# Performance work log

Hardware: AMD Instinct MI355X
Metric: run time of the kernel (lower is better)

The kernel has to match this reference:

```python
import jax, jax.numpy as jnp
import numpy as np

D_MODEL = 32   # channels arg = Mamba d_model
D_INNER = 32   # expand=1
D_STATE = 8
DT_RANK = 2    # ceil(32/16)
D_CONV = 4


def layer_norm(h, g, b, eps=1e-5):
    m = jnp.mean(h, axis=-1, keepdims=True)
    v = jnp.var(h, axis=-1, keepdims=True)
    return (h - m) * jax.lax.rsqrt(v + eps) * g + b


def causal_conv1d(h, w, b):
    # h: [B, d, L]; w: [d, K] depthwise; torch Conv1d(padding=K-1) truncated to first L
    out = jax.lax.conv_general_dilated(h, w[:, None, :], (1,), [(D_CONV - 1, 0)],
                                       dimension_numbers=('NCH', 'OIH', 'NCH'),
                                       feature_group_count=h.shape[1])
    return out + b[None, :, None]


def selective_scan(u, delta, A, Bm, Cm, D):
    # u, delta: [B, d, L]; A: [d, n]; Bm, Cm: [B, n, L]; D: [d]
    dA = jnp.exp(jnp.einsum('bdl,dn->lbdn', delta, A))       # [L, B, d, n]
    dBu = jnp.einsum('bdl,bnl,bdl->lbdn', delta, Bm, u)      # [L, B, d, n]
    Cseq = jnp.transpose(Cm, (2, 0, 1))                      # [L, B, n]
    h0 = jnp.zeros((u.shape[0], A.shape[0], A.shape[1]), u.dtype)

    def step(h, inp):
        dA_t, dBu_t, C_t = inp
        h = dA_t * h + dBu_t
        return h, jnp.einsum('bdn,bn->bd', h, C_t)

    _, ys = jax.lax.scan(step, h0, (dA, dBu, Cseq))          # ys: [L, B, d]
    return jnp.transpose(ys, (1, 2, 0)) + D[None, :, None] * u


def mamba_direction(xz, conv_w, conv_b, xproj_w, dtproj_w, dtproj_b, A_log, D):
    xh, z = jnp.split(xz, 2, axis=1)                         # each [B, d_inner, L]
    xh = jax.nn.silu(causal_conv1d(xh, conv_w, conv_b))
    x_dbl = jnp.einsum('bdl,kd->bkl', xh, xproj_w)           # [B, dt_rank+2n, L]
    dt, Bm, Cm = jnp.split(x_dbl, [DT_RANK, DT_RANK + D_STATE], axis=1)
    dt = jax.nn.softplus(jnp.einsum('brl,dr->bdl', dt, dtproj_w) + dtproj_b[None, :, None])
    y = selective_scan(xh, dt, -jnp.exp(A_log), Bm, Cm, D)
    return y * jax.nn.silu(z)


def forward(x, lin1_w, lin1_b, ln1_g, ln1_b, in_proj_w,
            conv_w_f, conv_b_f, xproj_w_f, dtproj_w_f, dtproj_b_f, A_log_f, D_f,
            conv_w_r, conv_b_r, xproj_w_r, dtproj_w_r, dtproj_b_r, A_log_r, D_r,
            out_proj_w, mnorm_g, mnorm_b, lin2_w, lin2_b):
    avg = jnp.mean(x, axis=(2, 3))                           # [B, C] adaptive avg pool
    mx = jnp.max(x, axis=(2, 3))                             # [B, C] adaptive max pool
    combined = jnp.stack([avg, mx], axis=-1)                 # [B, C, 2]
    h = combined @ lin1_w.T + lin1_b                         # [B, C, d_model]
    h = layer_norm(h, ln1_g, ln1_b)
    # bidirectional Mamba (bimamba v2) over sequence length L = C
    xz = jnp.einsum('blc,ec->bel', h, in_proj_w)             # [B, 2*d_inner, L]
    out_f = mamba_direction(xz, conv_w_f, conv_b_f, xproj_w_f, dtproj_w_f, dtproj_b_f, A_log_f, D_f)
    out_r = mamba_direction(xz[..., ::-1], conv_w_r, conv_b_r, xproj_w_r, dtproj_w_r, dtproj_b_r, A_log_r, D_r)[..., ::-1]
    out = (out_f + out_r) / 2.0                              # if_devide_out=True
    out = jnp.einsum('bdl,od->blo', out, out_proj_w)         # [B, L, d_model]
    out = layer_norm(out, mnorm_g, mnorm_b)                  # use_norm=True
    att = jax.nn.sigmoid(out @ lin2_w.T + lin2_b)            # [B, L, 1]
    return att[..., None] * 0.25 + 0.875                     # [B, C, 1, 1]


def setup_inputs() -> dict:
    key = jax.random.key(0)
    ks = jax.random.split(key, 12)
    B, C, H, W = 32, 512, 64, 64

    def rn(k, shape, s):
        return jax.random.normal(k, shape, jnp.float32) * s

    A_log = jnp.log(jnp.broadcast_to(jnp.arange(1, D_STATE + 1, dtype=jnp.float32), (D_INNER, D_STATE)))
    return {
        'x': jax.random.normal(ks[0], (B, C, H, W), jnp.float32),
        'lin1_w': rn(ks[1], (D_MODEL, 2), 0.5),
        'lin1_b': jnp.zeros((D_MODEL,), jnp.float32),
        'ln1_g': jnp.ones((D_MODEL,), jnp.float32),
        'ln1_b': jnp.zeros((D_MODEL,), jnp.float32),
        'in_proj_w': rn(ks[2], (2 * D_INNER, D_MODEL), 0.1),
        'conv_w_f': rn(ks[3], (D_INNER, D_CONV), 0.3),
        'conv_b_f': jnp.zeros((D_INNER,), jnp.float32),
        'xproj_w_f': rn(ks[4], (DT_RANK + 2 * D_STATE, D_INNER), 0.1),
        'dtproj_w_f': rn(ks[5], (D_INNER, DT_RANK), 0.5),
        'dtproj_b_f': jnp.full((D_INNER,), -4.6, jnp.float32),
        'A_log_f': A_log,
        'D_f': jnp.ones((D_INNER,), jnp.float32),
        'conv_w_r': rn(ks[6], (D_INNER, D_CONV), 0.3),
        'conv_b_r': jnp.zeros((D_INNER,), jnp.float32),
        'xproj_w_r': rn(ks[7], (DT_RANK + 2 * D_STATE, D_INNER), 0.1),
        'dtproj_w_r': rn(ks[8], (D_INNER, DT_RANK), 0.5),
        'dtproj_b_r': jnp.full((D_INNER,), -4.6, jnp.float32),
        'A_log_r': A_log,
        'D_r': jnp.ones((D_INNER,), jnp.float32),
        'out_proj_w': rn(ks[9], (D_MODEL, D_INNER), 0.1),
        'mnorm_g': jnp.ones((D_MODEL,), jnp.float32),
        'mnorm_b': jnp.zeros((D_MODEL,), jnp.float32),
        'lin2_w': rn(ks[10], (1, D_MODEL), 0.3),
        'lin2_b': jnp.zeros((1,), jnp.float32),
    }


def reference(x, lin1_w, lin1_b, ln1_g, ln1_b, in_proj_w,
              conv_w_f, conv_b_f, xproj_w_f, dtproj_w_f, dtproj_b_f, A_log_f, D_f,
              conv_w_r, conv_b_r, xproj_w_r, dtproj_w_r, dtproj_b_r, A_log_r, D_r,
              out_proj_w, mnorm_g, mnorm_b, lin2_w, lin2_b):
    return forward(x, lin1_w, lin1_b, ln1_g, ln1_b, in_proj_w,
                   conv_w_f, conv_b_f, xproj_w_f, dtproj_w_f, dtproj_b_f, A_log_f, D_f,
                   conv_w_r, conv_b_r, xproj_w_r, dtproj_w_r, dtproj_b_r, A_log_r, D_r,
                   out_proj_w, mnorm_g, mnorm_b, lin2_w, lin2_b)
```

## Files before the change

kernel.cpp:

```cpp
#include <hip/hip_runtime.h>
#include <math.h>

#define BB 32
#define CC 512
#define HW 4096
#define DM 32
#define DI 32
#define DS 8
#define KC 4

#define NCH 16
#define CHL 32

__device__ __forceinline__ float siluf(float x) {
    return x / (1.0f + __expf(-x));
}
__device__ __forceinline__ float softplusf(float x) {
    float ax = fabsf(x);
    return fmaxf(x, 0.0f) + log1pf(__expf(-ax));
}

__global__ __launch_bounds__(256) void poolproj_kernel(
    const float* __restrict__ x,
    const float* __restrict__ lin1_w, const float* __restrict__ lin1_b,
    const float* __restrict__ ln1_g, const float* __restrict__ ln1_b,
    const float* __restrict__ in_proj_w, float* __restrict__ xz)
{
    int bc = blockIdx.x;
    int b = bc >> 9, l = bc & 511;
    const float4* xp = reinterpret_cast<const float4*>(x + (size_t)bc * HW);
    int tid = threadIdx.x;

    __shared__ float sWp[64][33];
    __shared__ float ss[4], sm[4];
    __shared__ float h_s[DM];

    float s = 0.f, m = -INFINITY;
#pragma unroll
    for (int r = 0; r < 4; ++r) {
        float4 v = xp[r * 256 + tid];
        s += (v.x + v.y) + (v.z + v.w);
        m = fmaxf(m, fmaxf(fmaxf(v.x, v.y), fmaxf(v.z, v.w)));
    }
    for (int i = tid; i < 64 * DM; i += 256) sWp[i >> 5][i & 31] = in_proj_w[i];

    for (int off = 32; off > 0; off >>= 1) {
        s += __shfl_down(s, off);
        m = fmaxf(m, __shfl_down(m, off));
    }
    int wave = tid >> 6;
    if ((tid & 63) == 0) { ss[wave] = s; sm[wave] = m; }
    __syncthreads();

    if (tid < 32) {
        float S = (ss[0] + ss[1]) + (ss[2] + ss[3]);
        float M = fmaxf(fmaxf(sm[0], sm[1]), fmaxf(sm[2], sm[3]));
        float a = S * (1.0f / HW);
        int m_ = tid;
        float h = a * lin1_w[2 * m_] + M * lin1_w[2 * m_ + 1] + lin1_b[m_];
        float sum = h;
#pragma unroll
        for (int mask = 1; mask < 32; mask <<= 1) sum += __shfl_xor(sum, mask);
        float mean = sum * (1.0f / DM);
        float d = h - mean;
        float vs = d * d;
#pragma unroll
        for (int mask = 1; mask < 32; mask <<= 1) vs += __shfl_xor(vs, mask);
        float rs = rsqrtf(vs * (1.0f / DM) + 1e-5f);
        h_s[m_] = d * rs * ln1_g[m_] + ln1_b[m_];
    }
    __syncthreads();

    if (tid < 64) {
        int e = tid;
        float acc = 0.f;
#pragma unroll
        for (int m_ = 0; m_ < DM; ++m_) acc += h_s[m_] * sWp[e][m_];
        xz[(((size_t)b * 64 + e) << 9) + l] = acc;
    }
}

__global__ __launch_bounds__(256) void convscan1_kernel(
    const float* __restrict__ xz,
    const float* __restrict__ conv_w_f, const float* __restrict__ conv_b_f,
    const float* __restrict__ xproj_w_f, const float* __restrict__ dtproj_w_f,
    const float* __restrict__ dtproj_b_f,
    const float* __restrict__ conv_w_r, const float* __restrict__ conv_b_r,
    const float* __restrict__ xproj_w_r, const float* __restrict__ dtproj_w_r,
    const float* __restrict__ dtproj_b_r,
    const float* __restrict__ A_log_f, const float* __restrict__ A_log_r,
    float* __restrict__ u_g, float* __restrict__ dt_g,
    float* __restrict__ B_g, float* __restrict__ C_g,
    float* __restrict__ carrA, float* __restrict__ carrH)
{
    int bx = blockIdx.x;
    int bd = bx >> 4, j = bx & 15;
    int b = bd >> 1, dir = bd & 1;
    int tid = threadIdx.x;
    const float* cw = dir ? conv_w_r : conv_w_f;
    const float* cb = dir ? conv_b_r : conv_b_f;
    const float* xw = dir ? xproj_w_r : xproj_w_f;
    const float* dw = dir ? dtproj_w_r : dtproj_w_f;
    const float* db = dir ? dtproj_b_r : dtproj_b_f;
    const float* Alog = dir ? A_log_r : A_log_f;
    const float* xzb = xz + (size_t)b * 64 * 512;

    __shared__ float xt[32][39];
    __shared__ float xw_s[18][33];
    __shared__ float u_s[CHL][33];
    __shared__ float dt_s[CHL][33];
    __shared__ float B_s[CHL][9];
    __shared__ float C_s[CHL][9];
    __shared__ float dtr_s[CHL][2];

    for (int idx = tid; idx < 32 * 35; idx += 256) {
        int dd = idx / 35, t = idx - dd * 35;
        int sidx = j * CHL - 3 + t;
        float v = 0.f;
        if (sidx >= 0) {
            int orig = dir ? (511 - sidx) : sidx;
            v = xzb[(dd << 9) + orig];
        }
        xt[dd][t] = v;
    }
    for (int idx = tid; idx < 18 * 32; idx += 256)
        xw_s[idx >> 5][idx & 31] = xw[idx];
    __syncthreads();

    int l = tid >> 3, g8 = tid & 7;
#pragma unroll
    for (int i = 0; i < 4; ++i) {
        int dd = g8 * 4 + i;
        float acc = cb[dd];
#pragma unroll
        for (int k = 0; k < KC; ++k) acc += cw[dd * KC + k] * xt[dd][l + k];
        u_s[l][dd] = siluf(acc);
    }
    __syncthreads();

    for (int o = g8; o < 18; o += 8) {
        float acc = 0.f;
#pragma unroll
        for (int m_ = 0; m_ < 32; ++m_) acc += u_s[l][m_] * xw_s[o][m_];
        if (o < 2) dtr_s[l][o] = acc;
        else if (o < 10) B_s[l][o - 2] = acc;
        else             C_s[l][o - 10] = acc;
    }
    __syncthreads();

    size_t rowbase = ((size_t)bd * 512 + j * CHL) * 32;
    for (int idx = tid; idx < CHL * 32; idx += 256) {
        int ll = idx >> 5, dd = idx & 31;
        float v = dtr_s[ll][0] * dw[dd * 2] + dtr_s[ll][1] * dw[dd * 2 + 1] + db[dd];
        float sp = softplusf(v);
        dt_s[ll][dd] = sp;
        dt_g[rowbase + idx] = sp;
        u_g[rowbase + idx] = u_s[ll][dd];
    }
    size_t base8 = ((size_t)bd * 512 + j * CHL) * 8;
    if (tid < CHL * 8) {
        B_g[base8 + tid] = B_s[tid >> 3][tid & 7];
        C_g[base8 + tid] = C_s[tid >> 3][tid & 7];
    }
    __syncthreads();

    int dd = tid >> 3, nn = tid & 7;
    float Aa = -__expf(Alog[tid]);
    float ap = 1.f, h = 0.f;
#pragma unroll 4
    for (int sl = 0; sl < CHL; ++sl) {
        float dtv = dt_s[sl][dd];
        float uu  = u_s[sl][dd];
        float bm  = B_s[sl][nn];
        float dA  = __expf(dtv * Aa);
        ap *= dA;
        h = dA * h + dtv * uu * bm;
    }
    carrA[((size_t)bx << 8) + tid] = ap;
    carrH[((size_t)bx << 8) + tid] = h;
}

__global__ __launch_bounds__(128) void scan2final_kernel(
    const float* __restrict__ u_g, const float* __restrict__ dt_g,
    const float* __restrict__ B_g, const float* __restrict__ C_g,
    const float* __restrict__ carrA, const float* __restrict__ carrH,
    const float* __restrict__ A_log_f, const float* __restrict__ D_f,
    const float* __restrict__ A_log_r, const float* __restrict__ D_r,
    const float* __restrict__ xz,
    const float* __restrict__ out_proj_w, const float* __restrict__ mnorm_g,
    const float* __restrict__ mnorm_b, const float* __restrict__ lin2_w,
    const float* __restrict__ lin2_b, float* __restrict__ out)
{
    int bx = blockIdx.x;
    int b = bx >> 4, t = bx & 15;
    int tid = threadIdx.x;
    int dir = tid >> 6;
    int r = tid & 63;
    int dd = r >> 1, nh = r & 1, n0 = nh * 4;
    int bd = b * 2 + dir;
    int tt = dir ? (15 - t) : t;

    const float* Alog = dir ? A_log_r : A_log_f;
    const float* Dp   = dir ? D_r : D_f;

    float A0 = -__expf(Alog[dd * 8 + n0 + 0]);
    float A1 = -__expf(Alog[dd * 8 + n0 + 1]);
    float A2 = -__expf(Alog[dd * 8 + n0 + 2]);
    float A3 = -__expf(Alog[dd * 8 + n0 + 3]);
    float Dd = Dp[dd];

    float h0 = 0.f, h1 = 0.f, h2 = 0.f, h3 = 0.f;
    for (int jj = 0; jj < tt; ++jj) {
        size_t cbase = (((size_t)bd * NCH + jj) << 8) + dd * 8 + n0;
        float4 av = *reinterpret_cast<const float4*>(carrA + cbase);
        float4 hv = *reinterpret_cast<const float4*>(carrH + cbase);
        h0 = av.x * h0 + hv.x;
        h1 = av.y * h1 + hv.y;
        h2 = av.z * h2 + hv.z;
        h3 = av.w * h3 + hv.w;
    }

    __shared__ float y_s[2][2][CHL][33];

    size_t sb = (size_t)bd * 512 + tt * CHL;
#pragma unroll 4
    for (int sl = 0; sl < CHL; ++sl) {
        size_t s32 = (sb + sl) * 32 + dd;
        float dtv = dt_g[s32];
        float uu  = u_g[s32];
        float4 Bv = *reinterpret_cast<const float4*>(B_g + (sb + sl) * 8 + n0);
        float4 Cv = *reinterpret_cast<const float4*>(C_g + (sb + sl) * 8 + n0);
        float dtu = dtv * uu;
        h0 = __expf(dtv * A0) * h0 + dtu * Bv.x;
        h1 = __expf(dtv * A1) * h1 + dtu * Bv.y;
        h2 = __expf(dtv * A2) * h2 + dtu * Bv.z;
        h3 = __expf(dtv * A3) * h3 + dtu * Bv.w;
        float py = h0 * Cv.x + h1 * Cv.y + h2 * Cv.z + h3 * Cv.w;
        if (nh == 0) py += Dd * uu;
        int ll = dir ? (CHL - 1 - sl) : sl;
        y_s[dir][nh][ll][dd] = py;
    }
    __syncthreads();

    if (tid < CHL) {
        int lo = t * CHL + tid;
        float comb[DI];
#pragma unroll
        for (int d2 = 0; d2 < DI; ++d2) {
            float ys = y_s[0][0][tid][d2] + y_s[0][1][tid][d2]
                     + y_s[1][0][tid][d2] + y_s[1][1][tid][d2];
            float z = xz[(((size_t)(b * 64 + 32 + d2)) << 9) + lo];
            comb[d2] = 0.5f * ys * siluf(z);
        }
        float o[DM];
        float mean = 0.f;
#pragma unroll
        for (int oo = 0; oo < DM; ++oo) {
            float acc = 0.f;
#pragma unroll
            for (int d2 = 0; d2 < DI; ++d2) acc += comb[d2] * out_proj_w[oo * DI + d2];
            o[oo] = acc;
            mean += acc;
        }
        mean *= (1.0f / DM);
        float var = 0.f;
#pragma unroll
        for (int oo = 0; oo < DM; ++oo) { float df = o[oo] - mean; var += df * df; }
        var *= (1.0f / DM);
        float rs = rsqrtf(var + 1e-5f);
        float s = lin2_b[0];
#pragma unroll
        for (int oo = 0; oo < DM; ++oo) {
            float v = (o[oo] - mean) * rs * mnorm_g[oo] + mnorm_b[oo];
            s += v * lin2_w[oo];
        }
        float att = 1.0f / (1.0f + __expf(-s));
        out[(size_t)b * 512 + lo] = 0.25f * att + 0.875f;
    }
}

extern "C" void kernel_launch(void* const* d_in, const int* in_sizes, int n_in,
                              void* d_out, int out_size, void* d_ws, size_t ws_size,
                              hipStream_t stream)
{
    const float* x         = (const float*)d_in[0];
    const float* lin1_w    = (const float*)d_in[1];
    const float* lin1_b    = (const float*)d_in[2];
    const float* ln1_g     = (const float*)d_in[3];
    const float* ln1_b     = (const float*)d_in[4];
    const float* in_proj_w = (const float*)d_in[5];
    const float* conv_w_f  = (const float*)d_in[6];
    const float* conv_b_f  = (const float*)d_in[7];
    const float* xproj_w_f = (const float*)d_in[8];
    const float* dtproj_w_f= (const float*)d_in[9];
    const float* dtproj_b_f= (const float*)d_in[10];
    const float* A_log_f   = (const float*)d_in[11];
    const float* D_f       = (const float*)d_in[12];
    const float* conv_w_r  = (const float*)d_in[13];
    const float* conv_b_r  = (const float*)d_in[14];
    const float* xproj_w_r = (const float*)d_in[15];
    const float* dtproj_w_r= (const float*)d_in[16];
    const float* dtproj_b_r= (const float*)d_in[17];
    const float* A_log_r   = (const float*)d_in[18];
    const float* D_r       = (const float*)d_in[19];
    const float* out_proj_w= (const float*)d_in[20];
    const float* mnorm_g   = (const float*)d_in[21];
    const float* mnorm_b   = (const float*)d_in[22];
    const float* lin2_w    = (const float*)d_in[23];
    const float* lin2_b    = (const float*)d_in[24];

    float* ws   = (float*)d_ws;
    float* xz   = ws;
    float* u_g  = xz + 1048576;
    float* dt_g = u_g + 1048576;
    float* B_g  = dt_g + 1048576;
    float* C_g  = B_g + 262144;
    float* carrA= C_g + 262144;
    float* carrH= carrA + 262144;
    (void)ws_size; (void)in_sizes; (void)n_in; (void)out_size;

    poolproj_kernel<<<BB * CC, 256, 0, stream>>>(x, lin1_w, lin1_b, ln1_g, ln1_b, in_proj_w, xz);
    convscan1_kernel<<<BB * 2 * NCH, 256, 0, stream>>>(
        xz, conv_w_f, conv_b_f, xproj_w_f, dtproj_w_f, dtproj_b_f,
        conv_w_r, conv_b_r, xproj_w_r, dtproj_w_r, dtproj_b_r,
        A_log_f, A_log_r, u_g, dt_g, B_g, C_g, carrA, carrH);
    scan2final_kernel<<<BB * NCH, 128, 0, stream>>>(
        u_g, dt_g, B_g, C_g, carrA, carrH,
        A_log_f, D_f, A_log_r, D_r, xz,
        out_proj_w, mnorm_g, mnorm_b, lin2_w, lin2_b, (float*)d_out);
}
```

Baseline: 93.21 us.

## Pool per-wave rows, transpose xz layout, and batch carry loads in scan

The pooling kernel now launches 512 blocks, and each wave processes 8 rows of x with wave-level shuffles. This removes the 16384 tiny blocks and their block-wide syncs, and in_proj weights are loaded into shared memory once per 32 rows instead of once per row. The xz buffer layout changes from [B,64,L] to [B,L,64], so the projection writes are coalesced and the consumers read contiguous channel vectors. The carry-combine loop in the scan kernel loads four chunk carries at a time to expose memory-level parallelism. The trade-offs are fewer blocks for latency hiding in the 134MB streaming read, and transposed gather patterns in the conv kernel's load.

Measured after the change: 115.8 us. +24.3%, slower.

```diff
diff --git a/kernel.cpp b/kernel.cpp
--- a/kernel.cpp
+++ b/kernel.cpp
@@ -26,38 +26,31 @@
     const float* __restrict__ ln1_g, const float* __restrict__ ln1_b,
     const float* __restrict__ in_proj_w, float* __restrict__ xz)
 {
-    int bc = blockIdx.x;
-    int b = bc >> 9, l = bc & 511;
-    const float4* xp = reinterpret_cast<const float4*>(x + (size_t)bc * HW);
+    __shared__ float sWp[64][33];
     int tid = threadIdx.x;
-
-    __shared__ float sWp[64][33];
-    __shared__ float ss[4], sm[4];
-    __shared__ float h_s[DM];
-
-    float s = 0.f, m = -INFINITY;
-#pragma unroll
-    for (int r = 0; r < 4; ++r) {
-        float4 v = xp[r * 256 + tid];
-        s += (v.x + v.y) + (v.z + v.w);
-        m = fmaxf(m, fmaxf(fmaxf(v.x, v.y), fmaxf(v.z, v.w)));
-    }
     for (int i = tid; i < 64 * DM; i += 256) sWp[i >> 5][i & 31] = in_proj_w[i];
-
-    for (int off = 32; off > 0; off >>= 1) {
-        s += __shfl_down(s, off);
-        m = fmaxf(m, __shfl_down(m, off));
-    }
-    int wave = tid >> 6;
-    if ((tid & 63) == 0) { ss[wave] = s; sm[wave] = m; }
-    __syncthreads();
-
-    if (tid < 32) {
-        float S = (ss[0] + ss[1]) + (ss[2] + ss[3]);
-        float M = fmaxf(fmaxf(sm[0], sm[1]), fmaxf(sm[2], sm[3]));
-        float a = S * (1.0f / HW);
-        int m_ = tid;
-        float h = a * lin1_w[2 * m_] + M * lin1_w[2 * m_ + 1] + lin1_b[m_];
+    __syncthreads();
+
+    int wave = tid >> 6, lane = tid & 63;
+    int row0 = blockIdx.x * 32 + wave * 8;
+    for (int i = 0; i < 8; ++i) {
+        int row = row0 + i;
+        const float4* xp = reinterpret_cast<const float4*>(x + (size_t)row * HW);
+        float s = 0.f, mxv = -INFINITY;
+#pragma unroll
+        for (int k = 0; k < 16; ++k) {
+            float4 v = xp[k * 64 + lane];
+            s += (v.x + v.y) + (v.z + v.w);
+            mxv = fmaxf(mxv, fmaxf(fmaxf(v.x, v.y), fmaxf(v.z, v.w)));
+        }
+#pragma unroll
+        for (int off = 1; off < 64; off <<= 1) {
+            s += __shfl_xor(s, off);
+            mxv = fmaxf(mxv, __shfl_xor(mxv, off));
+        }
+        float a = s * (1.0f / HW);
+        int m_ = lane & 31;
+        float h = a * lin1_w[2 * m_] + mxv * lin1_w[2 * m_ + 1] + lin1_b[m_];
         float sum = h;
 #pragma unroll
         for (int mask = 1; mask < 32; mask <<= 1) sum += __shfl_xor(sum, mask);
@@ -67,16 +60,12 @@
 #pragma unroll
         for (int mask = 1; mask < 32; mask <<= 1) vs += __shfl_xor(vs, mask);
         float rs = rsqrtf(vs * (1.0f / DM) + 1e-5f);
-        h_s[m_] = d * rs * ln1_g[m_] + ln1_b[m_];
-    }
-    __syncthreads();
-
-    if (tid < 64) {
-        int e = tid;
+        float hn = d * rs * ln1_g[m_] + ln1_b[m_];
         float acc = 0.f;
 #pragma unroll
-        for (int m_ = 0; m_ < DM; ++m_) acc += h_s[m_] * sWp[e][m_];
-        xz[(((size_t)b * 64 + e) << 9) + l] = acc;
+        for (int mm = 0; mm < DM; ++mm)
+            acc += __shfl(hn, mm) * sWp[lane][mm];
+        xz[((size_t)row << 6) + lane] = acc;
     }
 }
 
@@ -103,7 +92,6 @@
     const float* dw = dir ? dtproj_w_r : dtproj_w_f;
     const float* db = dir ? dtproj_b_r : dtproj_b_f;
     const float* Alog = dir ? A_log_r : A_log_f;
-    const float* xzb = xz + (size_t)b * 64 * 512;
 
     __shared__ float xt[32][39];
     __shared__ float xw_s[18][33];
@@ -113,13 +101,13 @@
     __shared__ float C_s[CHL][9];
     __shared__ float dtr_s[CHL][2];
 
-    for (int idx = tid; idx < 32 * 35; idx += 256) {
-        int dd = idx / 35, t = idx - dd * 35;
+    for (int idx = tid; idx < 35 * 32; idx += 256) {
+        int t = idx >> 5, dd = idx & 31;
         int sidx = j * CHL - 3 + t;
         float v = 0.f;
         if (sidx >= 0) {
             int orig = dir ? (511 - sidx) : sidx;
-            v = xzb[(dd << 9) + orig];
+            v = xz[(((size_t)b * 512 + orig) << 6) + dd];
         }
         xt[dd][t] = v;
     }
@@ -210,14 +198,27 @@
     float Dd = Dp[dd];
 
     float h0 = 0.f, h1 = 0.f, h2 = 0.f, h3 = 0.f;
-    for (int jj = 0; jj < tt; ++jj) {
-        size_t cbase = (((size_t)bd * NCH + jj) << 8) + dd * 8 + n0;
-        float4 av = *reinterpret_cast<const float4*>(carrA + cbase);
-        float4 hv = *reinterpret_cast<const float4*>(carrH + cbase);
-        h0 = av.x * h0 + hv.x;
-        h1 = av.y * h1 + hv.y;
-        h2 = av.z * h2 + hv.z;
-        h3 = av.w * h3 + hv.w;
+    for (int g = 0; g < 4; ++g) {
+        int jbase = g * 4;
+        if (jbase >= tt) break;
+        float4 av[4], hv[4];
+#pragma unroll
+        for (int k = 0; k < 4; ++k) {
+            int jj = jbase + k;
+            int js = (jj < tt) ? jj : 0;
+            size_t cbase = (((size_t)bd * NCH + js) << 8) + dd * 8 + n0;
+            av[k] = *reinterpret_cast<const float4*>(carrA + cbase);
+            hv[k] = *reinterpret_cast<const float4*>(carrH + cbase);
+        }
+#pragma unroll
+        for (int k = 0; k < 4; ++k) {
+            if (jbase + k < tt) {
+                h0 = av[k].x * h0 + hv[k].x;
+                h1 = av[k].y * h1 + hv[k].y;
+                h2 = av[k].z * h2 + hv[k].z;
+                h3 = av[k].w * h3 + hv[k].w;
+            }
+        }
     }
 
     __shared__ float y_s[2][2][CHL][33];
@@ -244,13 +245,13 @@
 
     if (tid < CHL) {
         int lo = t * CHL + tid;
+        const float* zrow = xz + (((size_t)b * 512 + lo) << 6) + 32;
         float comb[DI];
 #pragma unroll
         for (int d2 = 0; d2 < DI; ++d2) {
             float ys = y_s[0][0][tid][d2] + y_s[0][1][tid][d2]
                      + y_s[1][0][tid][d2] + y_s[1][1][tid][d2];
-            float z = xz[(((size_t)(b * 64 + 32 + d2)) << 9) + lo];
-            comb[d2] = 0.5f * ys * siluf(z);
+            comb[d2] = 0.5f * ys * siluf(zrow[d2]);
         }
         float o[DM];
         float mean = 0.f;
@@ -319,7 +320,7 @@
     float* carrH= carrA + 262144;
     (void)ws_size; (void)in_sizes; (void)n_in; (void)out_size;
 
-    poolproj_kernel<<<BB * CC, 256, 0, stream>>>(x, lin1_w, lin1_b, ln1_g, ln1_b, in_proj_w, xz);
+    poolproj_kernel<<<512, 256, 0, stream>>>(x, lin1_w, lin1_b, ln1_g, ln1_b, in_proj_w, xz);
     convscan1_kernel<<<BB * 2 * NCH, 256, 0, stream>>>(
         xz, conv_w_f, conv_b_f, xproj_w_f, dtproj_w_f, dtproj_b_f,
         conv_w_r, conv_b_r, xproj_w_r, dtproj_w_r, dtproj_b_r,
```

## Split pooling from projection, transpose xz layout, widen final scan kernel

Applied to the files above, without the earlier changes.

The pooled reduction becomes its own lightweight kernel, and a separate projection kernel computes LayerNorm and in_proj with one wave per row. xz is stored position-major ([B, L, 64]), so the projection writes and the conv loads are coalesced. The final kernel now uses 512 threads, one per (dir, d, n): it stages u/dt/B/C/z and out_proj in shared memory, reduces over n with shuffles, and spreads the out_proj/LayerNorm/lin2 epilogue across all threads instead of 32. In exchange this adds a kernel launch and a round trip of the pooled values through global memory.

Result: faster. 86.76 us (-6.9%).

```diff
diff --git a/kernel.cpp b/kernel.cpp
--- a/kernel.cpp
+++ b/kernel.cpp
@@ -20,64 +20,66 @@
     return fmaxf(x, 0.0f) + log1pf(__expf(-ax));
 }
 
-__global__ __launch_bounds__(256) void poolproj_kernel(
-    const float* __restrict__ x,
+__global__ __launch_bounds__(256) void pool_kernel(const float* __restrict__ x,
+                                                   float* __restrict__ avg,
+                                                   float* __restrict__ mx) {
+    int bc = blockIdx.x;
+    const float4* xp = reinterpret_cast<const float4*>(x + (size_t)bc * HW);
+    int tid = threadIdx.x;
+    float s = 0.f, m = -INFINITY;
+#pragma unroll
+    for (int r = 0; r < 4; ++r) {
+        float4 v = xp[r * 256 + tid];
+        s += (v.x + v.y) + (v.z + v.w);
+        m = fmaxf(m, fmaxf(fmaxf(v.x, v.y), fmaxf(v.z, v.w)));
+    }
+    for (int off = 32; off > 0; off >>= 1) {
+        s += __shfl_down(s, off);
+        m = fmaxf(m, __shfl_down(m, off));
+    }
+    __shared__ float ss[4], sm[4];
+    int wave = tid >> 6;
+    if ((tid & 63) == 0) { ss[wave] = s; sm[wave] = m; }
+    __syncthreads();
+    if (tid == 0) {
+        float S = (ss[0] + ss[1]) + (ss[2] + ss[3]);
+        float M = fmaxf(fmaxf(sm[0], sm[1]), fmaxf(sm[2], sm[3]));
+        avg[bc] = S * (1.0f / HW);
+        mx[bc]  = M;
+    }
+}
+
+__global__ __launch_bounds__(256) void hproj_kernel(
+    const float* __restrict__ avg, const float* __restrict__ mx,
     const float* __restrict__ lin1_w, const float* __restrict__ lin1_b,
     const float* __restrict__ ln1_g, const float* __restrict__ ln1_b,
     const float* __restrict__ in_proj_w, float* __restrict__ xz)
 {
-    int bc = blockIdx.x;
-    int b = bc >> 9, l = bc & 511;
-    const float4* xp = reinterpret_cast<const float4*>(x + (size_t)bc * HW);
+    __shared__ float sWp[64][33];
     int tid = threadIdx.x;
-
-    __shared__ float sWp[64][33];
-    __shared__ float ss[4], sm[4];
-    __shared__ float h_s[DM];
-
-    float s = 0.f, m = -INFINITY;
-#pragma unroll
-    for (int r = 0; r < 4; ++r) {
-        float4 v = xp[r * 256 + tid];
-        s += (v.x + v.y) + (v.z + v.w);
-        m = fmaxf(m, fmaxf(fmaxf(v.x, v.y), fmaxf(v.z, v.w)));
-    }
     for (int i = tid; i < 64 * DM; i += 256) sWp[i >> 5][i & 31] = in_proj_w[i];
-
-    for (int off = 32; off > 0; off >>= 1) {
-        s += __shfl_down(s, off);
-        m = fmaxf(m, __shfl_down(m, off));
-    }
-    int wave = tid >> 6;
-    if ((tid & 63) == 0) { ss[wave] = s; sm[wave] = m; }
-    __syncthreads();
-
-    if (tid < 32) {
-        float S = (ss[0] + ss[1]) + (ss[2] + ss[3]);
-        float M = fmaxf(fmaxf(sm[0], sm[1]), fmaxf(sm[2], sm[3]));
-        float a = S * (1.0f / HW);
-        int m_ = tid;
-        float h = a * lin1_w[2 * m_] + M * lin1_w[2 * m_ + 1] + lin1_b[m_];
-        float sum = h;
-#pragma unroll
-        for (int mask = 1; mask < 32; mask <<= 1) sum += __shfl_xor(sum, mask);
-        float mean = sum * (1.0f / DM);
-        float d = h - mean;
-        float vs = d * d;
-#pragma unroll
-        for (int mask = 1; mask < 32; mask <<= 1) vs += __shfl_xor(vs, mask);
-        float rs = rsqrtf(vs * (1.0f / DM) + 1e-5f);
-        h_s[m_] = d * rs * ln1_g[m_] + ln1_b[m_];
-    }
-    __syncthreads();
-
-    if (tid < 64) {
-        int e = tid;
-        float acc = 0.f;
-#pragma unroll
-        for (int m_ = 0; m_ < DM; ++m_) acc += h_s[m_] * sWp[e][m_];
-        xz[(((size_t)b * 64 + e) << 9) + l] = acc;
-    }
+    __syncthreads();
+
+    int wave = tid >> 6, lane = tid & 63;
+    int row = blockIdx.x * 4 + wave;
+    float a = avg[row], M = mx[row];
+    int m_ = lane & 31;
+    float h = a * lin1_w[2 * m_] + M * lin1_w[2 * m_ + 1] + lin1_b[m_];
+    float sum = h;
+#pragma unroll
+    for (int mask = 1; mask < 32; mask <<= 1) sum += __shfl_xor(sum, mask);
+    float mean = sum * (1.0f / DM);
+    float d = h - mean;
+    float vs = d * d;
+#pragma unroll
+    for (int mask = 1; mask < 32; mask <<= 1) vs += __shfl_xor(vs, mask);
+    float rs = rsqrtf(vs * (1.0f / DM) + 1e-5f);
+    float hn = d * rs * ln1_g[m_] + ln1_b[m_];
+    float acc = 0.f;
+#pragma unroll
+    for (int mm = 0; mm < DM; ++mm)
+        acc += __shfl(hn, mm) * sWp[lane][mm];
+    xz[((size_t)row << 6) + lane] = acc;
 }
 
 __global__ __launch_bounds__(256) void convscan1_kernel(
@@ -103,7 +105,6 @@
     const float* dw = dir ? dtproj_w_r : dtproj_w_f;
     const float* db = dir ? dtproj_b_r : dtproj_b_f;
     const float* Alog = dir ? A_log_r : A_log_f;
-    const float* xzb = xz + (size_t)b * 64 * 512;
 
     __shared__ float xt[32][39];
     __shared__ float xw_s[18][33];
@@ -113,13 +114,13 @@
     __shared__ float C_s[CHL][9];
     __shared__ float dtr_s[CHL][2];
 
-    for (int idx = tid; idx < 32 * 35; idx += 256) {
-        int dd = idx / 35, t = idx - dd * 35;
+    for (int idx = tid; idx < 35 * 32; idx += 256) {
+        int t = idx >> 5, dd = idx & 31;
         int sidx = j * CHL - 3 + t;
         float v = 0.f;
         if (sidx >= 0) {
             int orig = dir ? (511 - sidx) : sidx;
-            v = xzb[(dd << 9) + orig];
+            v = xz[(((size_t)b * 512 + orig) << 6) + dd];
         }
         xt[dd][t] = v;
     }
@@ -180,7 +181,7 @@
     carrH[((size_t)bx << 8) + tid] = h;
 }
 
-__global__ __launch_bounds__(128) void scan2final_kernel(
+__global__ __launch_bounds__(512) void scan2final_kernel(
     const float* __restrict__ u_g, const float* __restrict__ dt_g,
     const float* __restrict__ B_g, const float* __restrict__ C_g,
     const float* __restrict__ carrA, const float* __restrict__ carrH,
@@ -194,88 +195,125 @@
     int bx = blockIdx.x;
     int b = bx >> 4, t = bx & 15;
     int tid = threadIdx.x;
-    int dir = tid >> 6;
-    int r = tid & 63;
-    int dd = r >> 1, nh = r & 1, n0 = nh * 4;
-    int bd = b * 2 + dir;
-    int tt = dir ? (15 - t) : t;
-
-    const float* Alog = dir ? A_log_r : A_log_f;
-    const float* Dp   = dir ? D_r : D_f;
-
-    float A0 = -__expf(Alog[dd * 8 + n0 + 0]);
-    float A1 = -__expf(Alog[dd * 8 + n0 + 1]);
-    float A2 = -__expf(Alog[dd * 8 + n0 + 2]);
-    float A3 = -__expf(Alog[dd * 8 + n0 + 3]);
-    float Dd = Dp[dd];
-
-    float h0 = 0.f, h1 = 0.f, h2 = 0.f, h3 = 0.f;
-    for (int jj = 0; jj < tt; ++jj) {
-        size_t cbase = (((size_t)bd * NCH + jj) << 8) + dd * 8 + n0;
-        float4 av = *reinterpret_cast<const float4*>(carrA + cbase);
-        float4 hv = *reinterpret_cast<const float4*>(carrH + cbase);
-        h0 = av.x * h0 + hv.x;
-        h1 = av.y * h1 + hv.y;
-        h2 = av.z * h2 + hv.z;
-        h3 = av.w * h3 + hv.w;
-    }
-
-    __shared__ float y_s[2][2][CHL][33];
-
-    size_t sb = (size_t)bd * 512 + tt * CHL;
+    int L0 = t * CHL;
+
+    __shared__ float u_s[2][CHL][33];
+    __shared__ float dt_s[2][CHL][33];
+    __shared__ float B_s[2][CHL][12];
+    __shared__ float C_s[2][CHL][12];
+    __shared__ float z_s[CHL][33];
+    __shared__ float y_s[2][CHL][33];
+    __shared__ float comb_s[CHL][33];
+    __shared__ float opw_s[DM][33];
+
+    for (int idx = tid; idx < 2 * CHL * 32; idx += 512) {
+        int dirw = idx >> 10;
+        int r2 = idx & 1023;
+        int sl = r2 >> 5, d = r2 & 31;
+        int bd = b * 2 + dirw;
+        int tc = dirw ? (15 - t) : t;
+        size_t g = ((size_t)bd * 512 + tc * CHL + sl) * 32 + d;
+        u_s[dirw][sl][d]  = u_g[g];
+        dt_s[dirw][sl][d] = dt_g[g];
+    }
+    {
+        int dirw = tid >> 8;
+        int r2 = tid & 255;
+        int sl = r2 >> 3, n = r2 & 7;
+        int bd = b * 2 + dirw;
+        int tc = dirw ? (15 - t) : t;
+        size_t g = ((size_t)bd * 512 + tc * CHL + sl) * 8 + n;
+        B_s[dirw][sl][n] = B_g[g];
+        C_s[dirw][sl][n] = C_g[g];
+    }
+    for (int idx = tid; idx < CHL * 32; idx += 512) {
+        int l = idx >> 5, d = idx & 31;
+        z_s[l][d] = xz[(((size_t)b * 512 + L0 + l) << 6) + 32 + d];
+        opw_s[idx >> 5][d] = out_proj_w[idx];
+    }
+    __syncthreads();
+
+    {
+        int dir = tid >> 8;
+        int r = tid & 255;
+        int d = r >> 3, n = r & 7;
+        int bd = b * 2 + dir;
+        int tt = dir ? (15 - t) : t;
+        const float* Alog = dir ? A_log_r : A_log_f;
+        const float* Dp   = dir ? D_r : D_f;
+        float A  = -__expf(Alog[r]);
+        float Dd = Dp[d];
+
+        float h = 0.f;
+        for (int g4 = 0; g4 < 4; ++g4) {
+            int jbase = g4 * 4;
+            if (jbase >= tt) break;
+            float av[4], hv[4];
+#pragma unroll
+            for (int k = 0; k < 4; ++k) {
+                int jj = jbase + k;
+                int js = (jj < tt) ? jj : 0;
+                size_t cb2 = (((size_t)bd * NCH + js) << 8) + r;
+                av[k] = carrA[cb2];
+                hv[k] = carrH[cb2];
+            }
+#pragma unroll
+            for (int k = 0; k < 4; ++k)
+                if (jbase + k < tt) h = av[k] * h + hv[k];
+        }
+
 #pragma unroll 4
-    for (int sl = 0; sl < CHL; ++sl) {
-        size_t s32 = (sb + sl) * 32 + dd;
-        float dtv = dt_g[s32];
-        float uu  = u_g[s32];
-        float4 Bv = *reinterpret_cast<const float4*>(B_g + (sb + sl) * 8 + n0);
-        float4 Cv = *reinterpret_cast<const float4*>(C_g + (sb + sl) * 8 + n0);
-        float dtu = dtv * uu;
-        h0 = __expf(dtv * A0) * h0 + dtu * Bv.x;
-        h1 = __expf(dtv * A1) * h1 + dtu * Bv.y;
-        h2 = __expf(dtv * A2) * h2 + dtu * Bv.z;
-        h3 = __expf(dtv * A3) * h3 + dtu * Bv.w;
-        float py = h0 * Cv.x + h1 * Cv.y + h2 * Cv.z + h3 * Cv.w;
-        if (nh == 0) py += Dd * uu;
-        int ll = dir ? (CHL - 1 - sl) : sl;
-        y_s[dir][nh][ll][dd] = py;
-    }
-    __syncthreads();
-
-    if (tid < CHL) {
-        int lo = t * CHL + tid;
-        float comb[DI];
-#pragma unroll
-        for (int d2 = 0; d2 < DI; ++d2) {
-            float ys = y_s[0][0][tid][d2] + y_s[0][1][tid][d2]
-                     + y_s[1][0][tid][d2] + y_s[1][1][tid][d2];
-            float z = xz[(((size_t)(b * 64 + 32 + d2)) << 9) + lo];
-            comb[d2] = 0.5f * ys * siluf(z);
-        }
-        float o[DM];
-        float mean = 0.f;
-#pragma unroll
-        for (int oo = 0; oo < DM; ++oo) {
-            float acc = 0.f;
-#pragma unroll
-            for (int d2 = 0; d2 < DI; ++d2) acc += comb[d2] * out_proj_w[oo * DI + d2];
-            o[oo] = acc;
-            mean += acc;
-        }
-        mean *= (1.0f / DM);
-        float var = 0.f;
-#pragma unroll
-        for (int oo = 0; oo < DM; ++oo) { float df = o[oo] - mean; var += df * df; }
-        var *= (1.0f / DM);
-        float rs = rsqrtf(var + 1e-5f);
-        float s = lin2_b[0];
-#pragma unroll
-        for (int oo = 0; oo < DM; ++oo) {
-            float v = (o[oo] - mean) * rs * mnorm_g[oo] + mnorm_b[oo];
-            s += v * lin2_w[oo];
-        }
-        float att = 1.0f / (1.0f + __expf(-s));
-        out[(size_t)b * 512 + lo] = 0.25f * att + 0.875f;
+        for (int sl = 0; sl < CHL; ++sl) {
+            float dtv = dt_s[dir][sl][d];
+            float uu  = u_s[dir][sl][d];
+            float bm  = B_s[dir][sl][n];
+            float cm  = C_s[dir][sl][n];
+            h = __expf(dtv * A) * h + dtv * uu * bm;
+            float py = h * cm;
+            py += __shfl_xor(py, 1);
+            py += __shfl_xor(py, 2);
+            py += __shfl_xor(py, 4);
+            if (n == 0) {
+                int ll = dir ? (CHL - 1 - sl) : sl;
+                y_s[dir][ll][d] = py + Dd * uu;
+            }
+        }
+    }
+    __syncthreads();
+
+    for (int idx = tid; idx < CHL * 32; idx += 512) {
+        int l = idx >> 5, d = idx & 31;
+        comb_s[l][d] = 0.5f * (y_s[0][l][d] + y_s[1][l][d]) * siluf(z_s[l][d]);
+    }
+    __syncthreads();
+
+    {
+        int l = tid >> 4, k = tid & 15;
+        float oa = 0.f, ob = 0.f;
+#pragma unroll
+        for (int d = 0; d < DI; ++d) {
+            float c = comb_s[l][d];
+            oa += c * opw_s[k][d];
+            ob += c * opw_s[k + 16][d];
+        }
+        float sum = oa + ob;
+#pragma unroll
+        for (int mask = 1; mask < 16; mask <<= 1) sum += __shfl_xor(sum, mask);
+        float mean = sum * (1.0f / DM);
+        float da = oa - mean, db2 = ob - mean;
+        float vs = da * da + db2 * db2;
+#pragma unroll
+        for (int mask = 1; mask < 16; mask <<= 1) vs += __shfl_xor(vs, mask);
+        float rs = rsqrtf(vs * (1.0f / DM) + 1e-5f);
+        float va = da * rs * mnorm_g[k] + mnorm_b[k];
+        float vb = db2 * rs * mnorm_g[k + 16] + mnorm_b[k + 16];
+        float sv = va * lin2_w[k] + vb * lin2_w[k + 16];
+#pragma unroll
+        for (int mask = 1; mask < 16; mask <<= 1) sv += __shfl_xor(sv, mask);
+        if (k == 0) {
+            float att = 1.0f / (1.0f + __expf(-(sv + lin2_b[0])));
+            out[(size_t)b * 512 + L0 + l] = 0.25f * att + 0.875f;
+        }
     }
 }
 
@@ -310,7 +348,9 @@
     const float* lin2_b    = (const float*)d_in[24];
 
     float* ws   = (float*)d_ws;
-    float* xz   = ws;
+    float* avg  = ws;
+    float* mx   = ws + 16384;
+    float* xz   = ws + 32768;
     float* u_g  = xz + 1048576;
     float* dt_g = u_g + 1048576;
     float* B_g  = dt_g + 1048576;
@@ -319,12 +359,13 @@
     float* carrH= carrA + 262144;
     (void)ws_size; (void)in_sizes; (void)n_in; (void)out_size;
 
-    poolproj_kernel<<<BB * CC, 256, 0, stream>>>(x, lin1_w, lin1_b, ln1_g, ln1_b, in_proj_w, xz);
+    pool_kernel<<<BB * CC, 256, 0, stream>>>(x, avg, mx);
+    hproj_kernel<<<4096, 256, 0, stream>>>(avg, mx, lin1_w, lin1_b, ln1_g, ln1_b, in_proj_w, xz);
     convscan1_kernel<<<BB * 2 * NCH, 256, 0, stream>>>(
         xz, conv_w_f, conv_b_f, xproj_w_f, dtproj_w_f, dtproj_b_f,
         conv_w_r, conv_b_r, xproj_w_r, dtproj_w_r, dtproj_b_r,
         A_log_f, A_log_r, u_g, dt_g, B_g, C_g, carrA, carrH);
-    scan2final_kernel<<<BB * NCH, 128, 0, stream>>>(
+    scan2final_kernel<<<BB * NCH, 512, 0, stream>>>(
         u_g, dt_g, B_g, C_g, carrA, carrH,
         A_log_f, D_f, A_log_r, D_r, xz,
         out_proj_w, mnorm_g, mnorm_b, lin2_w, lin2_b, (float*)d_out);
```
